# Kernel tuning notes

Measured on AMD Instinct MI355X. Metric: run time of the kernel, lower is better.

The kernel has to match this reference:

```python
import jax, jax.numpy as jnp
import numpy as np

HEADS, KV_HEADS, HEAD_DIM = 32, 8, 64


def apply_rope(x, cos, sin):
    # x: [b,h,s,d], cos/sin: [s, d//2]; pairs are interleaved (even/odd)
    c = cos[None, None, :, :]
    s = sin[None, None, :, :]
    x1 = x[..., 0::2]
    x2 = x[..., 1::2]
    xn = x1 * c - x2 * s
    yn = x1 * s + x2 * c
    return jnp.stack([xn, yn], axis=-1).reshape(x.shape)


def setup_inputs() -> dict:
    key = jax.random.key(0)
    ks = jax.random.split(key, 7)
    b, s, h = 1, 2048, 2048
    return {
        "x": jax.random.normal(ks[0], (b, s, h), jnp.float32),
        "cos": jax.random.normal(ks[1], (s, HEAD_DIM // 2), jnp.float32),
        "sin": jax.random.normal(ks[2], (s, HEAD_DIM // 2), jnp.float32),
        "Wq": jax.random.normal(ks[3], (h, HEADS * HEAD_DIM), jnp.float32) * 0.02,
        "Wk": jax.random.normal(ks[4], (h, KV_HEADS * HEAD_DIM), jnp.float32) * 0.02,
        "Wv": jax.random.normal(ks[5], (h, KV_HEADS * HEAD_DIM), jnp.float32) * 0.02,
        "Wo": jax.random.normal(ks[6], (HEADS * HEAD_DIM, h), jnp.float32) * 0.02,
    }


def reference(x, cos, sin, Wq, Wk, Wv, Wo):
    b, seq, hidden = x.shape
    Q = x @ Wq  # [b,s,H*d]
    K = x @ Wk  # [b,s,Kh*d]
    V = x @ Wv
    q = Q.reshape(b, seq, HEADS, HEAD_DIM).transpose(0, 2, 1, 3)      # b h s d
    k = K.reshape(b, seq, KV_HEADS, HEAD_DIM).transpose(0, 2, 1, 3)   # b k s d
    v = V.reshape(b, seq, KV_HEADS, HEAD_DIM).transpose(0, 2, 1, 3)
    r = HEADS // KV_HEADS
    # einops 'b k s d -> b (r k) s d': tile kv-head block r times
    k = jnp.tile(k, (1, r, 1, 1))
    v = jnp.tile(v, (1, r, 1, 1))
    q = apply_rope(q, cos, sin)
    k = apply_rope(k, cos, sin)
    scale = 1.0 / jnp.sqrt(jnp.float32(HEAD_DIM))
    qk = jnp.einsum('bhqd,bhkd->bhqk', q, k) * scale
    mask = jnp.triu(jnp.full((seq, seq), -jnp.inf, qk.dtype), k=1)
    attn = jax.nn.softmax(qk + mask, axis=-1)
    av = jnp.einsum('bhqk,bhkd->bhqd', attn, v)
    av = av.transpose(0, 2, 1, 3).reshape(b, seq, HEADS * HEAD_DIM)
    return av @ Wo
```

## Files before the change

kernel.cpp:

```cpp
#include <hip/hip_runtime.h>

typedef unsigned short u16;
typedef __attribute__((ext_vector_type(4))) float f32x4;
typedef __attribute__((ext_vector_type(16))) float f32x16;
typedef __attribute__((ext_vector_type(8))) __bf16 bf16x8;
typedef __attribute__((ext_vector_type(2))) __bf16 bf16x2;

#define HEADS 32
#define KV_HEADS 8
#define HD 64
#define SEQ 2048
#define HID 2048
#define NQK 3072
#define QSCALE (0.125f * 1.4426950408889634f)
#define OCH 2097152u

#define AS1 __attribute__((address_space(1)))
#define AS3 __attribute__((address_space(3)))

__device__ __forceinline__ u16 f2bf(float f) {
  unsigned u = __float_as_uint(f);
  u += 0x7FFFu + ((u >> 16) & 1u);
  return (u16)(u >> 16);
}

__device__ __forceinline__ unsigned pk2(float a, float b) {
  union { bf16x2 h; unsigned u; } c;
  c.h[0] = (__bf16)a; c.h[1] = (__bf16)b;
  return c.u;
}

__device__ __forceinline__ float bflo(unsigned u) {
  return __uint_as_float(u << 16);
}
__device__ __forceinline__ float bfhi(unsigned u) {
  return __uint_as_float(u & 0xFFFF0000u);
}

__device__ __forceinline__ void load16_to_lds(const void* g, void* l) {
  __builtin_amdgcn_global_load_lds((AS1 void*)(void*)g, (AS3 void*)l, 16, 0, 0);
}

__global__ __launch_bounds__(256) void k_f2b(const float* __restrict__ in,
                                             u16* __restrict__ out, int n4) {
  int i = blockIdx.x * 256 + threadIdx.x;
  if (i >= n4) return;
  float4 v = ((const float4*)in)[i];
  ushort4 o;
  o.x = f2bf(v.x); o.y = f2bf(v.y); o.z = f2bf(v.z); o.w = f2bf(v.w);
  ((ushort4*)out)[i] = o;
}

__global__ __launch_bounds__(256) void k_tconv(const float* __restrict__ in, int ldi,
                                               u16* __restrict__ out, int ldo) {
  __shared__ float tile[32][33];
  int c0 = blockIdx.x * 32, r0 = blockIdx.y * 32;
  int col = threadIdx.x & 31, rw = threadIdx.x >> 5;
#pragma unroll
  for (int i = 0; i < 4; i++)
    tile[rw + i * 8][col] = in[(size_t)(r0 + rw + i * 8) * ldi + c0 + col];
  __syncthreads();
#pragma unroll
  for (int i = 0; i < 4; i++)
    out[(size_t)(c0 + rw + i * 8) * ldo + r0 + col] = f2bf(tile[col][rw + i * 8]);
}


__device__ __forceinline__ void stage8(const u16* Ap, const u16* Bp, u16* AsX,
                                       u16* BsX, int tid, int K, int koff) {
#pragma unroll
  for (int i = 0; i < 4; i++) {
    load16_to_lds(Ap + (size_t)(i * 32) * K + koff, AsX + (i * 256 + tid) * 8);
    load16_to_lds(Bp + (size_t)(i * 32) * K + koff, BsX + (i * 256 + tid) * 8);
  }
}

__device__ __forceinline__ void frag16(const u16* Asb, const u16* Bsb,
                                       const int aoff[4][2], const int boff[4][2],
                                       f32x4 acc[4][4]) {
#pragma unroll
  for (int kk = 0; kk < 2; kk++) {
    bf16x8 a[4], b[4];
#pragma unroll
    for (int i = 0; i < 4; i++)
      a[i] = *(const bf16x8*)((const char*)Asb + aoff[i][kk]);
#pragma unroll
    for (int j = 0; j < 4; j++)
      b[j] = *(const bf16x8*)((const char*)Bsb + boff[j][kk]);
#pragma unroll
    for (int i = 0; i < 4; i++)
#pragma unroll
      for (int j = 0; j < 4; j++)
        acc[i][j] = __builtin_amdgcn_mfma_f32_16x16x32_bf16(a[i], b[j], acc[i][j], 0, 0, 0);
  }
}

#define TILE_STEP(AsX, BsX, tnext)                              \
  do {                                                          \
    asm volatile("s_waitcnt vmcnt(8)" ::: "memory");            \
    __builtin_amdgcn_sched_barrier(0);                          \
    __builtin_amdgcn_s_barrier();                               \
    frag16(AsX, BsX, aoff, boff, acc);                          \
    __builtin_amdgcn_sched_barrier(0);                          \
    __builtin_amdgcn_s_barrier();                               \
    stage8(Ap, Bp, AsX, BsX, tid, K, (tnext) * 64);             \
    __builtin_amdgcn_sched_barrier(0);                          \
  } while (0)

#define TILE_TAIL(AsX, BsX, n)                                  \
  do {                                                          \
    asm volatile("s_waitcnt vmcnt(" #n ")" ::: "memory");       \
    __builtin_amdgcn_sched_barrier(0);                          \
    __builtin_amdgcn_s_barrier();                               \
    frag16(AsX, BsX, aoff, boff, acc);                          \
  } while (0)

__global__ __launch_bounds__(256) void k_gemm(const u16* __restrict__ A,
                                              const u16* __restrict__ Bt,
                                              float* __restrict__ C,
                                              int M, int N, int K) {
  __shared__ u16 smem[32768];
  u16* As0 = smem;          u16* As1 = smem + 8192;
  u16* Bs0 = smem + 16384;  u16* Bs1 = smem + 24576;
  int tid = threadIdx.x;
  int m0 = blockIdx.x * 128, n0 = blockIdx.y * 128;
  int l = tid & 63, w = tid >> 6;
  int lr = l & 15, lg = l >> 4;
  int wr = (w >> 1) * 64, wc = (w & 1) * 64;
  f32x4 acc[4][4] = {};
  int r8 = tid >> 3;
  int sx = (tid & 7) ^ (r8 & 7);
  const u16* Ap = A + (size_t)(m0 + r8) * K + sx * 8;
  const u16* Bp = Bt + (size_t)(n0 + r8) * K + sx * 8;
  int aoff[4][2], boff[4][2];
#pragma unroll
  for (int i = 0; i < 4; i++) {
    int ra = wr + i * 16 + lr;
    int rb = wc + i * 16 + lr;
#pragma unroll
    for (int kk = 0; kk < 2; kk++) {
      aoff[i][kk] = ra * 128 + (((lg + kk * 4) ^ (ra & 7)) << 4);
      boff[i][kk] = rb * 128 + (((lg + kk * 4) ^ (rb & 7)) << 4);
    }
  }
  stage8(Ap, Bp, As0, Bs0, tid, K, 0);
  stage8(Ap, Bp, As1, Bs1, tid, K, 64);
#pragma unroll 1
  for (int t = 0; t < 30; t += 2) {
    TILE_STEP(As0, Bs0, t + 2);
    TILE_STEP(As1, Bs1, t + 3);
  }
  TILE_TAIL(As0, Bs0, 8);
  TILE_TAIL(As1, Bs1, 0);

#pragma unroll
  for (int i = 0; i < 4; i++)
#pragma unroll
    for (int j = 0; j < 4; j++)
#pragma unroll
      for (int r = 0; r < 4; r++)
        C[(size_t)(m0 + wr + i * 16 + lg * 4 + r) * N + n0 + wc + j * 16 + lr] =
            acc[i][j][r];
}


__device__ __forceinline__ void stageQ(const u16* Ap, const u16* Bp, u16* S,
                                       int tid, int koff) {
#pragma unroll
  for (int i = 0; i < 2; i++)
    load16_to_lds(Ap + (size_t)(i * 32) * HID + koff, S + (i * 256 + tid) * 8);
#pragma unroll
  for (int i = 0; i < 6; i++)
    load16_to_lds(Bp + (size_t)(i * 32) * HID + koff, S + 4096 + (i * 256 + tid) * 8);
}

__device__ __forceinline__ void frag26(const u16* Sb, const int aoff[2][2],
                                       const int boff[6][2], f32x4 acc[2][6]) {
#pragma unroll
  for (int kk = 0; kk < 2; kk++) {
    bf16x8 a[2], b[6];
#pragma unroll
    for (int i = 0; i < 2; i++)
      a[i] = *(const bf16x8*)((const char*)Sb + aoff[i][kk]);
#pragma unroll
    for (int j = 0; j < 6; j++)
      b[j] = *(const bf16x8*)((const char*)Sb + 8192 + boff[j][kk]);
    __builtin_amdgcn_s_setprio(1);
#pragma unroll
    for (int i = 0; i < 2; i++)
#pragma unroll
      for (int j = 0; j < 6; j++)
        acc[i][j] = __builtin_amdgcn_mfma_f32_16x16x32_bf16(a[i], b[j], acc[i][j], 0, 0, 0);
    __builtin_amdgcn_s_setprio(0);
  }
}

#define QK_STEP(Sc, tnext)                                      \
  do {                                                          \
    asm volatile("s_waitcnt vmcnt(8)" ::: "memory");            \
    __builtin_amdgcn_sched_barrier(0);                          \
    __builtin_amdgcn_s_barrier();                               \
    frag26(Sc, aoff, boff, acc);                                \
    __builtin_amdgcn_sched_barrier(0);                          \
    __builtin_amdgcn_s_barrier();                               \
    stageQ(Ap, Bp, Sc, tid, (tnext) * 64);                      \
    __builtin_amdgcn_sched_barrier(0);                          \
  } while (0)

#define QK_TAIL(Sc, n)                                          \
  do {                                                          \
    asm volatile("s_waitcnt vmcnt(" #n ")" ::: "memory");       \
    __builtin_amdgcn_sched_barrier(0);                          \
    __builtin_amdgcn_s_barrier();                               \
    frag26(Sc, aoff, boff, acc);                                \
  } while (0)

__global__ __launch_bounds__(256) void k_gemm_qkv(const u16* __restrict__ A,
                                                  const u16* __restrict__ Bt,
                                                  const float* __restrict__ cosp,
                                                  const float* __restrict__ sinp,
                                                  u16* __restrict__ qbuf,
                                                  u16* __restrict__ kbuf,
                                                  u16* __restrict__ vtb) {
  __shared__ u16 smem[32768];
  u16* S0 = smem;
  u16* S1 = smem + 16384;
  u16* Ts = smem;
  int tid = threadIdx.x;
  int bid = blockIdx.x;
  int wg = (bid & 7) * 64 + (bid >> 3);
  int m0 = (wg & 31) * 64, n0 = (wg >> 5) * 192;
  int l = tid & 63, w = tid >> 6;
  int lr = l & 15, lg = l >> 4;
  int wr = (w >> 1) * 32, wc = (w & 1) * 96;
  f32x4 acc[2][6] = {};
  int r8 = tid >> 3;
  int sx = (tid & 7) ^ (r8 & 7);
  const u16* Ap = A + (size_t)(m0 + r8) * HID + sx * 8;
  const u16* Bp = Bt + (size_t)(n0 + r8) * HID + sx * 8;
  int aoff[2][2], boff[6][2];
#pragma unroll
  for (int i = 0; i < 2; i++) {
    int ra = wr + i * 16 + lr;
#pragma unroll
    for (int kk = 0; kk < 2; kk++)
      aoff[i][kk] = ra * 128 + (((lg + kk * 4) ^ (ra & 7)) << 4);
  }
#pragma unroll
  for (int j = 0; j < 6; j++) {
    int rb = wc + j * 16 + lr;
#pragma unroll
    for (int kk = 0; kk < 2; kk++)
      boff[j][kk] = rb * 128 + (((lg + kk * 4) ^ (rb & 7)) << 4);
  }

  stageQ(Ap, Bp, S0, tid, 0);
  stageQ(Ap, Bp, S1, tid, 64);
#pragma unroll 1
  for (int t = 0; t < 30; t += 2) {
    QK_STEP(S0, t + 2);
    QK_STEP(S1, t + 3);
  }
  QK_TAIL(S0, 8);
  QK_TAIL(S1, 0);

  int odd = lr & 1;
#pragma unroll
  for (int j = 0; j < 6; j++) {
    int colf = n0 + wc + j * 16;
    if (colf < 2560) {
      bool isQ = colf < 2048;
      float scale = isQ ? QSCALE : 1.0f;
      u16* base = isQ ? qbuf + (size_t)(colf >> 6) * SEQ * HD
                      : kbuf + (size_t)((colf - 2048) >> 6) * SEQ * HD;
      int ch = colf & 63;
      int ii = (ch >> 1) + (lr >> 1);
#pragma unroll
      for (int i = 0; i < 2; i++)
#pragma unroll
        for (int r = 0; r < 4; r++) {
          float v = acc[i][j][r];
          float vp = __shfl_xor(v, 1, 64);
          int sr = m0 + wr + i * 16 + lg * 4 + r;
          float cs = cosp[sr * 32 + ii], sn = sinp[sr * 32 + ii];
          float x1 = odd ? vp : v, x2 = odd ? v : vp;
          float o = odd ? (x1 * sn + x2 * cs) : (x1 * cs - x2 * sn);
          base[(size_t)sr * HD + ch + lr] = f2bf(o * scale);
        }
    }
  }
  if (n0 + 192 > 2560) {
    __syncthreads();
#pragma unroll
    for (int j = 0; j < 6; j++) {
      int colf = n0 + wc + j * 16;
      if (colf >= 2560) {
#pragma unroll
        for (int i = 0; i < 2; i++)
#pragma unroll
          for (int r = 0; r < 4; r++) {
            int cB = wc + j * 16 + lr, rB = wr + i * 16 + lg * 4 + r;
            *(u16*)((char*)Ts + cB * 128 + ((rB * 2) ^ ((cB & 7) << 4))) =
                f2bf(acc[i][j][r]);
          }
      }
    }
    __syncthreads();
    int half = tid & 1;
#pragma unroll
    for (int p = 0; p < 2; p++) {
      int c = p * 128 + (tid >> 1);
      if (c < 192 && n0 + c >= 2560) {
        int col = n0 + c;
        int kvh = (col - 2560) >> 6, d = col & 63;
        u16* dst = vtb + (size_t)kvh * HD * SEQ + (size_t)d * SEQ + m0 + half * 32;
        const char* src = (const char*)Ts + c * 128;
        int cs7 = (c & 7) << 4;
#pragma unroll
        for (int q = 0; q < 4; q++)
          *(uint4*)(dst + q * 8) = *(const uint4*)(src + ((half * 64 + q * 16) ^ cs7));
      }
    }
  }
}

__global__ __launch_bounds__(256) void k_flash2(const u16* __restrict__ qb,
                                                const u16* __restrict__ kb,
                                                const u16* __restrict__ vt,
                                                unsigned* __restrict__ Opart,
                                                float2* __restrict__ ml) {
  __shared__ u16 Ks[2][64 * 64];
  __shared__ u16 Vs[2][64 * 64];
  int bid = blockIdx.x;
  int c = bid & 1;
  int b5 = bid >> 1;
  int h = b5 & 31;
  int qi = b5 >> 5;
  int qblk = (SEQ / 128) - 1 - qi;
  int kvh = h & 7;
  int tid = threadIdx.x, w = tid >> 6, l = tid & 63;
  int lq = l & 31, hi = l >> 5;
  const u16* qh = qb + (size_t)h * SEQ * HD;
  const u16* kh = kb + (size_t)kvh * SEQ * HD;
  const u16* vh = vt + (size_t)kvh * HD * SEQ;
  int wq0 = qblk * 128 + w * 32;
  int qg = wq0 + lq;

  bf16x8 qf[4];
#pragma unroll
  for (int ds = 0; ds < 4; ds++)
    qf[ds] = *(const bf16x8*)(qh + (size_t)qg * HD + ds * 16 + hi * 8);

  f32x16 acc[2] = {};
  float m_r = -__builtin_inff(), l_r = 0.f;

  int srow = tid >> 2, c4 = tid & 3, swz = (srow & 7) << 4;
  int sd0 = srow * 128 + ((c4 * 32) ^ swz);
  int sd1 = srow * 128 + ((c4 * 32 + 16) ^ swz);
  const int kt0 = c * (qblk + 1), kt1 = kt0 + qblk + 1;

  {
    const u16* ksrc = kh + (size_t)(kt0 * 64 + srow) * HD + c4 * 16;
    const u16* vsrc = vh + (size_t)srow * SEQ + kt0 * 64 + c4 * 16;
    uint4 a0 = *(const uint4*)(ksrc), a1 = *(const uint4*)(ksrc + 8);
    uint4 b0 = *(const uint4*)(vsrc), b1 = *(const uint4*)(vsrc + 8);
    *(uint4*)((char*)Ks[0] + sd0) = a0; *(uint4*)((char*)Ks[0] + sd1) = a1;
    *(uint4*)((char*)Vs[0] + sd0) = b0; *(uint4*)((char*)Vs[0] + sd1) = b1;
  }
  __syncthreads();

  uint4 kr0, kr1, vr0, vr1;
  int lswz = (lq & 7) << 4;
  for (int kt = kt0; kt < kt1; kt++) {
    int b = (kt - kt0) & 1;
    if (kt + 1 < kt1) {
      const u16* ksrc = kh + (size_t)((kt + 1) * 64 + srow) * HD + c4 * 16;
      const u16* vsrc = vh + (size_t)srow * SEQ + (kt + 1) * 64 + c4 * 16;
      kr0 = *(const uint4*)(ksrc); kr1 = *(const uint4*)(ksrc + 8);
      vr0 = *(const uint4*)(vsrc); vr1 = *(const uint4*)(vsrc + 8);
    }

    if (kt * 64 <= wq0 + 31) {
      f32x16 sT[2] = {};
      const char* kbase = (const char*)Ks[b];
      __builtin_amdgcn_s_setprio(1);
#pragma unroll
      for (int t = 0; t < 2; t++) {
#pragma unroll
        for (int ds = 0; ds < 4; ds++) {
          bf16x8 kf = *(const bf16x8*)(kbase + (t * 32 + lq) * 128 +
                                       ((ds * 32 + hi * 16) ^ lswz));
          sT[t] = __builtin_amdgcn_mfma_f32_32x32x16_bf16(kf, qf[ds], sT[t], 0, 0, 0);
        }
      }
      __builtin_amdgcn_s_setprio(0);

      if (kt * 64 + 63 > wq0) {
#pragma unroll
        for (int t = 0; t < 2; t++)
#pragma unroll
          for (int r = 0; r < 16; r++) {
            int kg = kt * 64 + t * 32 + (r & 3) + 8 * (r >> 2) + 4 * hi;
            if (kg > qg) sT[t][r] = -__builtin_inff();
          }
      }

      float pmax = sT[0][0];
#pragma unroll
      for (int r = 1; r < 16; r++) pmax = fmaxf(pmax, sT[0][r]);
#pragma unroll
      for (int r = 0; r < 16; r++) pmax = fmaxf(pmax, sT[1][r]);
      pmax = fmaxf(pmax, __shfl_xor(pmax, 32, 64));

      if (!__all(pmax <= m_r + 8.f)) {
        float mn = fmaxf(m_r, pmax);
        float scl = __builtin_amdgcn_exp2f(m_r - mn);
        l_r *= scl;
        acc[0] *= scl;
        acc[1] *= scl;
        m_r = mn;
      }

      float ss = 0.f;
#pragma unroll
      for (int t = 0; t < 2; t++)
#pragma unroll
        for (int r = 0; r < 16; r++) {
          float p = __builtin_amdgcn_exp2f(sT[t][r] - m_r);
          sT[t][r] = p;
          ss += p;
        }
      ss += __shfl_xor(ss, 32, 64);
      l_r += ss;

      const char* vbase = (const char*)Vs[b];
#pragma unroll
      for (int t = 0; t < 2; t++) {
        unsigned cp[4][2];
#pragma unroll
        for (int m = 0; m < 4; m++) {
          cp[m][0] = pk2(sT[t][4 * m + 0], sT[t][4 * m + 1]);
          cp[m][1] = pk2(sT[t][4 * m + 2], sT[t][4 * m + 3]);
        }
#pragma unroll
        for (int kl = 0; kl < 2; kl++) {
          unsigned s0 = hi ? cp[2 * kl][0] : cp[2 * kl + 1][0];
          unsigned s1 = hi ? cp[2 * kl][1] : cp[2 * kl + 1][1];
          unsigned r0 = (unsigned)__shfl_xor((int)s0, 32, 64);
          unsigned r1 = (unsigned)__shfl_xor((int)s1, 32, 64);
          union { unsigned u[4]; bf16x8 v; } pa;
          pa.u[0] = hi ? r0 : cp[2 * kl][0];
          pa.u[1] = hi ? r1 : cp[2 * kl][1];
          pa.u[2] = hi ? cp[2 * kl + 1][0] : r0;
          pa.u[3] = hi ? cp[2 * kl + 1][1] : r1;
          int ks = t * 2 + kl;
          __builtin_amdgcn_s_setprio(1);
#pragma unroll
          for (int dt = 0; dt < 2; dt++) {
            bf16x8 vb = *(const bf16x8*)(vbase + (dt * 32 + lq) * 128 +
                                         ((ks * 32 + hi * 16) ^ lswz));
            acc[dt] = __builtin_amdgcn_mfma_f32_32x32x16_bf16(vb, pa.v, acc[dt], 0, 0, 0);
          }
          __builtin_amdgcn_s_setprio(0);
        }
      }
    }

    if (kt + 1 < kt1) {
      *(uint4*)((char*)Ks[b ^ 1] + sd0) = kr0;
      *(uint4*)((char*)Ks[b ^ 1] + sd1) = kr1;
      *(uint4*)((char*)Vs[b ^ 1] + sd0) = vr0;
      *(uint4*)((char*)Vs[b ^ 1] + sd1) = vr1;
    }
    __syncthreads();
  }

  unsigned* op = Opart + (size_t)c * OCH + ((size_t)(b5 * 4 + w) * 16) * 64;
#pragma unroll
  for (int dt = 0; dt < 2; dt++)
#pragma unroll
    for (int j = 0; j < 8; j++)
      op[(dt * 8 + j) * 64 + l] = pk2(acc[dt][2 * j], acc[dt][2 * j + 1]);
  if (!hi)
    ml[c * (HEADS * SEQ) + h * SEQ + wq0 + lq] = make_float2(m_r, l_r);
}

__global__ __launch_bounds__(256) void k_merge(const unsigned* __restrict__ Opart,
                                               const float2* __restrict__ ml,
                                               u16* __restrict__ av) {
  __shared__ u16 Ts[8192];
  int bid = blockIdx.x;
  int h = bid & 31, qblk = bid >> 5;
  int b5 = ((SEQ / 128 - 1 - qblk) << 5) | h;
  int tid = threadIdx.x, w = tid >> 6, l = tid & 63;
  int lq = l & 31, hi = l >> 5;
  int wq0 = qblk * 128 + w * 32;

  float2 ml0 = ml[h * SEQ + wq0 + lq];
  float2 ml1 = ml[HEADS * SEQ + h * SEQ + wq0 + lq];
  float m = fmaxf(ml0.x, ml1.x);
  float f0 = __builtin_amdgcn_exp2f(ml0.x - m);
  float f1 = __builtin_amdgcn_exp2f(ml1.x - m);
  float inv = 1.0f / (ml0.y * f0 + ml1.y * f1);

  const unsigned* op0 = Opart + ((size_t)(b5 * 4 + w) * 16) * 64;
  const unsigned* op1 = op0 + OCH;
  f32x16 acc[2];
#pragma unroll
  for (int dt = 0; dt < 2; dt++)
#pragma unroll
    for (int j = 0; j < 8; j++) {
      unsigned a0 = op0[(dt * 8 + j) * 64 + l];
      unsigned a1 = op1[(dt * 8 + j) * 64 + l];
      acc[dt][2 * j] = bflo(a0) * f0 + bflo(a1) * f1;
      acc[dt][2 * j + 1] = bfhi(a0) * f0 + bfhi(a1) * f1;
    }

  int lswz = (lq & 7) << 4;
  char* wbase = (char*)Ts + w * 4096;
#pragma unroll
  for (int dt = 0; dt < 2; dt++)
#pragma unroll
    for (int m4 = 0; m4 < 4; m4++) {
      int r0 = 4 * m4;
      uint2 pr;
      pr.x = pk2(acc[dt][r0 + 0] * inv, acc[dt][r0 + 1] * inv);
      pr.y = pk2(acc[dt][r0 + 2] * inv, acc[dt][r0 + 3] * inv);
      int byte = lq * 128 + ((dt * 64 + m4 * 16 + hi * 8) ^ lswz);
      *(uint2*)(wbase + byte) = pr;
    }
  __syncthreads();
  int q2 = l >> 1, cH = l & 1;
  int qswz = (q2 & 7) << 4;
#pragma unroll
  for (int i = 0; i < 4; i++) {
    uint4 d = *(const uint4*)(wbase + q2 * 128 + ((cH * 64 + i * 16) ^ qswz));
    *(uint4*)(av + (size_t)(wq0 + q2) * HID + h * HD + cH * 32 + i * 8) = d;
  }
}

extern "C" void kernel_launch(void* const* d_in, const int* in_sizes, int n_in,
                              void* d_out, int out_size, void* d_ws, size_t ws_size,
                              hipStream_t stream) {
  (void)in_sizes; (void)n_in; (void)out_size; (void)ws_size;
  const float* x = (const float*)d_in[0];
  const float* cosp = (const float*)d_in[1];
  const float* sinp = (const float*)d_in[2];
  const float* Wq = (const float*)d_in[3];
  const float* Wk = (const float*)d_in[4];
  const float* Wv = (const float*)d_in[5];
  const float* Wo = (const float*)d_in[6];
  float* out = (float*)d_out;
  char* ws = (char*)d_ws;

  u16* xb = (u16*)(ws);
  float2* mlb = (float2*)(ws);
  u16* Wqkv = (u16*)(ws + ((size_t)8 << 20));
  u16* WoT = (u16*)(ws + ((size_t)20 << 20));
  u16* qbuf = (u16*)(ws + ((size_t)28 << 20));
  u16* kbuf = (u16*)(ws + ((size_t)36 << 20));
  u16* vtb = (u16*)(ws + ((size_t)38 << 20));
  u16* av = (u16*)(ws + ((size_t)40 << 20));
  unsigned* Opart = (unsigned*)(ws + ((size_t)48 << 20));

  k_f2b<<<(SEQ * HID / 4 + 255) / 256, 256, 0, stream>>>(x, xb, SEQ * HID / 4);
  k_tconv<<<dim3(HID / 32, HID / 32), 256, 0, stream>>>(Wq, HID, Wqkv, HID);
  k_tconv<<<dim3(512 / 32, HID / 32), 256, 0, stream>>>(Wk, 512, Wqkv + (size_t)2048 * HID, HID);
  k_tconv<<<dim3(512 / 32, HID / 32), 256, 0, stream>>>(Wv, 512, Wqkv + (size_t)2560 * HID, HID);
  k_tconv<<<dim3(HID / 32, HID / 32), 256, 0, stream>>>(Wo, HID, WoT, HID);
  k_gemm_qkv<<<512, 256, 0, stream>>>(xb, Wqkv, cosp, sinp, qbuf, kbuf, vtb);
  k_flash2<<<(SEQ / 128) * HEADS * 2, 256, 0, stream>>>(qbuf, kbuf, vtb, Opart, mlb);
  k_merge<<<(SEQ / 128) * HEADS, 256, 0, stream>>>(Opart, mlb, av);
  k_gemm<<<dim3(SEQ / 128, HID / 128), 256, 0, stream>>>(av, WoT, out, SEQ, HID, HID);
}
```

Measured before the change: 124.1 us.

## Merge weight transpose launches and widen QKV GEMM tile to 64x384

```diff
diff --git a/kernel.cpp b/kernel.cpp
--- a/kernel.cpp
+++ b/kernel.cpp
@@ -51,10 +51,29 @@
   ((ushort4*)out)[i] = o;
 }
 
-__global__ __launch_bounds__(256) void k_tconv(const float* __restrict__ in, int ldi,
-                                               u16* __restrict__ out, int ldo) {
+__global__ __launch_bounds__(256) void k_tconv4(const float* __restrict__ Wq,
+                                                const float* __restrict__ Wk,
+                                                const float* __restrict__ Wv,
+                                                const float* __restrict__ Wo,
+                                                u16* __restrict__ Wqkv,
+                                                u16* __restrict__ WoT) {
   __shared__ float tile[32][33];
-  int c0 = blockIdx.x * 32, r0 = blockIdx.y * 32;
+  int bid = blockIdx.x;
+  const float* in; u16* out; int ldi, cx, cy;
+  if (bid < 4096) {
+    in = Wq; out = Wqkv; ldi = 2048; cx = bid & 63; cy = bid >> 6;
+  } else if (bid < 5120) {
+    int b = bid - 4096;
+    in = Wk; out = Wqkv + (size_t)2048 * 2048; ldi = 512; cx = b & 15; cy = b >> 4;
+  } else if (bid < 6144) {
+    int b = bid - 5120;
+    in = Wv; out = Wqkv + (size_t)2560 * 2048; ldi = 512; cx = b & 15; cy = b >> 4;
+  } else {
+    int b = bid - 6144;
+    in = Wo; out = WoT; ldi = 2048; cx = b & 63; cy = b >> 6;
+  }
+  const int ldo = 2048;
+  int c0 = cx * 32, r0 = cy * 32;
   int col = threadIdx.x & 31, rw = threadIdx.x >> 5;
 #pragma unroll
   for (int i = 0; i < 4; i++)
@@ -164,14 +183,12 @@
 }
 
 
-__device__ __forceinline__ void stageQ(const u16* Ap, const u16* Bp, u16* S,
-                                       int tid, int koff) {
-#pragma unroll
-  for (int i = 0; i < 2; i++)
-    load16_to_lds(Ap + (size_t)(i * 32) * HID + koff, S + (i * 256 + tid) * 8);
+__device__ __forceinline__ void stageQ8(const u16* Ap, const u16* Bp, u16* S,
+                                        int tid, int koff) {
+  load16_to_lds(Ap + koff, S + tid * 8);
 #pragma unroll
   for (int i = 0; i < 6; i++)
-    load16_to_lds(Bp + (size_t)(i * 32) * HID + koff, S + 4096 + (i * 256 + tid) * 8);
+    load16_to_lds(Bp + (size_t)(i * 64) * HID + koff, S + 4096 + (i * 512 + tid) * 8);
 }
 
 __device__ __forceinline__ void frag26(const u16* Sb, const int aoff[2][2],
@@ -197,13 +214,13 @@
 
 #define QK_STEP(Sc, tnext)                                      \
   do {                                                          \
-    asm volatile("s_waitcnt vmcnt(8)" ::: "memory");            \
+    asm volatile("s_waitcnt vmcnt(7)" ::: "memory");            \
     __builtin_amdgcn_sched_barrier(0);                          \
     __builtin_amdgcn_s_barrier();                               \
     frag26(Sc, aoff, boff, acc);                                \
     __builtin_amdgcn_sched_barrier(0);                          \
     __builtin_amdgcn_s_barrier();                               \
-    stageQ(Ap, Bp, Sc, tid, (tnext) * 64);                      \
+    stageQ8(Ap, Bp, Sc, tid, (tnext) * 64);                     \
     __builtin_amdgcn_sched_barrier(0);                          \
   } while (0)
 
@@ -215,24 +232,24 @@
     frag26(Sc, aoff, boff, acc);                                \
   } while (0)
 
-__global__ __launch_bounds__(256) void k_gemm_qkv(const u16* __restrict__ A,
-                                                  const u16* __restrict__ Bt,
-                                                  const float* __restrict__ cosp,
-                                                  const float* __restrict__ sinp,
-                                                  u16* __restrict__ qbuf,
-                                                  u16* __restrict__ kbuf,
-                                                  u16* __restrict__ vtb) {
-  __shared__ u16 smem[32768];
+__global__ __launch_bounds__(512, 2) void k_gemm_qkv(const u16* __restrict__ A,
+                                                     const u16* __restrict__ Bt,
+                                                     const float* __restrict__ cosp,
+                                                     const float* __restrict__ sinp,
+                                                     u16* __restrict__ qbuf,
+                                                     u16* __restrict__ kbuf,
+                                                     u16* __restrict__ vtb) {
+  __shared__ u16 smem[57344];
   u16* S0 = smem;
-  u16* S1 = smem + 16384;
+  u16* S1 = smem + 28672;
   u16* Ts = smem;
   int tid = threadIdx.x;
   int bid = blockIdx.x;
-  int wg = (bid & 7) * 64 + (bid >> 3);
-  int m0 = (wg & 31) * 64, n0 = (wg >> 5) * 192;
+  int wg = (bid & 7) * 32 + (bid >> 3);
+  int m0 = (wg & 31) * 64, n0 = (wg >> 5) * 384;
   int l = tid & 63, w = tid >> 6;
   int lr = l & 15, lg = l >> 4;
-  int wr = (w >> 1) * 32, wc = (w & 1) * 96;
+  int wr = (w >> 2) * 32, wc = (w & 3) * 96;
   f32x4 acc[2][6] = {};
   int r8 = tid >> 3;
   int sx = (tid & 7) ^ (r8 & 7);
@@ -254,14 +271,14 @@
       boff[j][kk] = rb * 128 + (((lg + kk * 4) ^ (rb & 7)) << 4);
   }
 
-  stageQ(Ap, Bp, S0, tid, 0);
-  stageQ(Ap, Bp, S1, tid, 64);
+  stageQ8(Ap, Bp, S0, tid, 0);
+  stageQ8(Ap, Bp, S1, tid, 64);
 #pragma unroll 1
   for (int t = 0; t < 30; t += 2) {
     QK_STEP(S0, t + 2);
     QK_STEP(S1, t + 3);
   }
-  QK_TAIL(S0, 8);
+  QK_TAIL(S0, 7);
   QK_TAIL(S1, 0);
 
   int odd = lr & 1;
@@ -289,7 +306,7 @@
         }
     }
   }
-  if (n0 + 192 > 2560) {
+  if (n0 + 384 > 2560) {
     __syncthreads();
 #pragma unroll
     for (int j = 0; j < 6; j++) {
@@ -309,8 +326,8 @@
     int half = tid & 1;
 #pragma unroll
     for (int p = 0; p < 2; p++) {
-      int c = p * 128 + (tid >> 1);
-      if (c < 192 && n0 + c >= 2560) {
+      int c = p * 256 + (tid >> 1);
+      if (c < 384 && n0 + c >= 2560) {
         int col = n0 + c;
         int kvh = (col - 2560) >> 6, d = col & 63;
         u16* dst = vtb + (size_t)kvh * HD * SEQ + (size_t)d * SEQ + m0 + half * 32;
@@ -564,11 +581,8 @@
   unsigned* Opart = (unsigned*)(ws + ((size_t)48 << 20));
 
   k_f2b<<<(SEQ * HID / 4 + 255) / 256, 256, 0, stream>>>(x, xb, SEQ * HID / 4);
-  k_tconv<<<dim3(HID / 32, HID / 32), 256, 0, stream>>>(Wq, HID, Wqkv, HID);
-  k_tconv<<<dim3(512 / 32, HID / 32), 256, 0, stream>>>(Wk, 512, Wqkv + (size_t)2048 * HID, HID);
-  k_tconv<<<dim3(512 / 32, HID / 32), 256, 0, stream>>>(Wv, 512, Wqkv + (size_t)2560 * HID, HID);
-  k_tconv<<<dim3(HID / 32, HID / 32), 256, 0, stream>>>(Wo, HID, WoT, HID);
-  k_gemm_qkv<<<512, 256, 0, stream>>>(xb, Wqkv, cosp, sinp, qbuf, kbuf, vtb);
+  k_tconv4<<<10240, 256, 0, stream>>>(Wq, Wk, Wv, Wo, Wqkv, WoT);
+  k_gemm_qkv<<<256, 512, 0, stream>>>(xb, Wqkv, cosp, sinp, qbuf, kbuf, vtb);
   k_flash2<<<(SEQ / 128) * HEADS * 2, 256, 0, stream>>>(qbuf, kbuf, vtb, Opart, mlb);
   k_merge<<<(SEQ / 128) * HEADS, 256, 0, stream>>>(Opart, mlb, av);
   k_gemm<<<dim3(SEQ / 128, HID / 128), 256, 0, stream>>>(av, WoT, out, SEQ, HID, HID);
```

Result: faster. 120.9 us (-2.5%).
